# Optimization experiments

Hardware: AMD Instinct MI355X
Metric: run time of the kernel (lower is better)

Reference implementation:

```python
import jax, jax.numpy as jnp
import numpy as np
from jax import lax

B, T, V, H, L = 4096, 256, 256, 20, 15  # batch, seq_len, one_hot_size, hidden_dim, MAX_LABEL


def setup_inputs() -> dict:
    key = jax.random.key(0)
    k0, k1, k2, k3 = jax.random.split(key, 4)
    return {
        "x": jax.random.randint(k0, (B, T), 0, V, dtype=jnp.int32),
        "drop_rate": jnp.float32(0.0),
        "kernel": jax.random.normal(k1, (V, 3 * H), dtype=jnp.float32) * 0.05,
        "recurrent_kernel": jax.random.normal(k2, (H, 3 * H), dtype=jnp.float32) * 0.05,
        "bias": jnp.zeros((2, 3 * H), dtype=jnp.float32),  # [input_bias, recurrent_bias] (reset_after=True)
        "dense_w": jax.random.normal(k3, (H, L), dtype=jnp.float32) * 0.05,
        "dense_b": jnp.zeros((L,), dtype=jnp.float32),
    }


def reference(x, drop_rate, kernel, recurrent_kernel, bias, dense_w, dense_b):
    # one_hot(x, 256) @ kernel is exactly a row-gather of kernel: same math, no 1GB one-hot.
    bi, br = bias[0], bias[1]
    xW = kernel[x] + bi  # [B, T, 3H]

    def step(h, xw_t):
        # Keras GRUCell, reset_after=True, gate order (z, r, h)
        hU = h @ recurrent_kernel + br                      # [B, 3H]
        xz, xr, xh = jnp.split(xw_t, 3, axis=-1)
        hz, hr, hh = jnp.split(hU, 3, axis=-1)
        z = jax.nn.sigmoid(xz + hz)
        r = jax.nn.sigmoid(xr + hr)
        h_cand = jnp.tanh(xh + r * hh)
        h_new = z * h + (1.0 - z) * h_cand
        return h_new, None

    h0 = jnp.zeros((x.shape[0], recurrent_kernel.shape[0]), dtype=kernel.dtype)
    hT, _ = lax.scan(step, h0, jnp.swapaxes(xW, 0, 1))     # scan over time, final state [B, H]

    # tf.nn.dropout: keep with prob 1-rate, scale kept values by 1/(1-rate).
    keep = 1.0 - drop_rate
    mask = jax.random.uniform(jax.random.key(42), hT.shape) >= drop_rate
    h_drop = jnp.where(mask, hT / keep, 0.0)

    logits = h_drop @ dense_w + dense_b                     # [B, 15]
    return logits
```

## Files before the change

### kernel.cpp

```cpp
#include <hip/hip_runtime.h>


#define BB 4096
#define TT 256
#define VV 256
#define HH 20
#define G3 60
#define LL 15
#define L2E 1.44269504088896340736f

typedef int v4i __attribute__((ext_vector_type(4)));
typedef int v2i __attribute__((ext_vector_type(2)));

static __device__ __forceinline__ unsigned short f2bf(float f) {
    union { float f; unsigned int i; } c; c.f = f;
    unsigned int x = c.i;
    return (unsigned short)((x + 0x7FFFu + ((x >> 16) & 1u)) >> 16);
}
static __device__ __forceinline__ unsigned pack2bf(float a, float b) {
    return (unsigned)f2bf(a) | ((unsigned)f2bf(b) << 16);
}
static __device__ __forceinline__ float fast_rcp(float x) {
#if __has_builtin(__builtin_amdgcn_rcpf)
    return __builtin_amdgcn_rcpf(x);
#else
    return 1.0f / x;
#endif
}
static __device__ __forceinline__ float dot2bf(unsigned a, unsigned b, float c) {
    float d;
    asm("v_dot2_f32_bf16 %0, %1, %2, %3" : "=v"(d) : "v"(a), "v"(b), "v"(c));
    return d;
}
static __device__ __forceinline__ unsigned cvtpk(float a, float b) {
    unsigned r;
    asm("v_cvt_pk_bf16_f32 %0, %1, %2" : "=v"(r) : "v"(a), "v"(b));
    return r;
}
static __device__ __forceinline__ float exp2i(float x) {
    float r; asm("v_exp_f32 %0, %1" : "=v"(r) : "v"(x)); return r;
}
static __device__ __forceinline__ void h_exchange(unsigned waddr, unsigned hbf,
                                                  unsigned raddr,
                                                  v4i& p0, v4i& p1, v2i& p2) {
    asm volatile(
        "ds_write_b16 %3, %4\n\t"
        "ds_read_b128 %0, %5\n\t"
        "ds_read_b128 %1, %5 offset:16\n\t"
        "ds_read_b64 %2, %5 offset:32\n\t"
        "s_waitcnt lgkmcnt(0)"
        : "=&v"(p0), "=&v"(p1), "=&v"(p2)
        : "v"(waddr), "v"(hbf), "v"(raddr));
}

__global__ __launch_bounds__(64, 2) void gru_kernel(
    const int* __restrict__ x,
    const float* __restrict__ kernelW,
    const float* __restrict__ rkernel,
    const float* __restrict__ bias,
    const float* __restrict__ dense_w,
    const float* __restrict__ dense_b,
    float* __restrict__ out)
{
    __shared__ __align__(16) unsigned short hbuf[80];

    const int lane = threadIdx.x;
    const int g3a  = lane / 20;
    const int g3   = (lane < 60) ? g3a : 0;
    const int j    = lane - g3a * 20;
    const bool active = (lane < 60);
    const long b  = (long)blockIdx.x * 3 + g3;
    const long bc = (b < BB) ? b : (BB - 1);

    if (lane < 40) *(int*)&hbuf[lane * 2] = 0;

    const unsigned hbase = (unsigned)(size_t)&hbuf[0];
    const unsigned waddr = active ? (hbase + 48u * (unsigned)g3a + 2u * (unsigned)j)
                                  : (hbase + 144u + 2u * (unsigned)(lane - 60));
    const unsigned raddr = hbase + 48u * (unsigned)g3;

    unsigned Uz[10], Ur[10], Uh[10];
    #pragma unroll
    for (int q = 0; q < 10; ++q) {
        Uz[q] = pack2bf(rkernel[(2*q)*G3 + j]        * (-L2E),
                        rkernel[(2*q+1)*G3 + j]      * (-L2E));
        Ur[q] = pack2bf(rkernel[(2*q)*G3 + HH + j]   * (-L2E),
                        rkernel[(2*q+1)*G3 + HH + j] * (-L2E));
        Uh[q] = pack2bf(rkernel[(2*q)*G3 + 2*HH + j]   * (2.0f*L2E),
                        rkernel[(2*q+1)*G3 + 2*HH + j] * (2.0f*L2E));
    }
    const float bzc = (bias[j]        + bias[G3 + j])      * (-L2E);
    const float brc = (bias[HH + j]   + bias[G3 + HH + j]) * (-L2E);
    const float bhi =  bias[2*HH + j]                      * (2.0f*L2E);
    const float brh =  bias[G3 + 2*HH + j]                 * (2.0f*L2E);

    const int* xrow = x + bc * TT;

    const int xv0 = xrow[0];
    const float* kw0 = kernelW + xv0 * G3;
    float cz = fmaf(kw0[j],        -L2E,     bzc);
    float cr = fmaf(kw0[HH + j],   -L2E,     brc);
    float ch = fmaf(kw0[2*HH + j], 2.0f*L2E, bhi);
    int xvA = xrow[1];

    float hmine = 0.0f;
    unsigned hbf = 0;

    for (int t = 0; t < TT; ++t) {
        const float* kwn = kernelW + xvA * G3;
        const float lz = kwn[j];
        const float lr = kwn[HH + j];
        const float lh = kwn[2*HH + j];
        const int xvB = xrow[(t + 2 < TT) ? (t + 2) : (TT - 1)];

        v4i p0, p1; v2i p2;
        h_exchange(waddr, hbf, raddr, p0, p1, p2);
        const unsigned hp[10] = { (unsigned)p0.x, (unsigned)p0.y, (unsigned)p0.z,
                                  (unsigned)p0.w, (unsigned)p1.x, (unsigned)p1.y,
                                  (unsigned)p1.z, (unsigned)p1.w, (unsigned)p2.x,
                                  (unsigned)p2.y };

        float za = cz,  ra = cr,  ha = brh;
        float zb = 0.f, rb = 0.f, hb = 0.f;
        #pragma unroll
        for (int q = 0; q < 5; ++q) {
            za = dot2bf(hp[q], Uz[q], za);
            ra = dot2bf(hp[q], Ur[q], ra);
            ha = dot2bf(hp[q], Uh[q], ha);
        }
        #pragma unroll
        for (int q = 5; q < 10; ++q) {
            zb = dot2bf(hp[q], Uz[q], zb);
            rb = dot2bf(hp[q], Ur[q], rb);
            hb = dot2bf(hp[q], Uh[q], hb);
        }

        const float z  = fast_rcp(1.0f + exp2i(za + zb));
        const float r  = fast_rcp(1.0f + exp2i(ra + rb));
        const float yh = fmaf(r, ha + hb, ch);
        const float hc = fmaf(-2.0f, fast_rcp(1.0f + exp2i(yh)), 1.0f);
        hmine = hc + z * (hmine - hc);
        hbf = cvtpk(hmine, hmine);

        cz = fmaf(lz, -L2E,     bzc);
        cr = fmaf(lr, -L2E,     brc);
        ch = fmaf(lh, 2.0f*L2E, bhi);
        xvA = xvB;
    }

    v4i p0, p1; v2i p2;
    h_exchange(waddr, hbf, raddr, p0, p1, p2);
    const unsigned fp[10] = { (unsigned)p0.x, (unsigned)p0.y, (unsigned)p0.z,
                              (unsigned)p0.w, (unsigned)p1.x, (unsigned)p1.y,
                              (unsigned)p1.z, (unsigned)p1.w, (unsigned)p2.x,
                              (unsigned)p2.y };
    float hf[HH];
    #pragma unroll
    for (int q = 0; q < 10; ++q) {
        hf[2*q]   = __uint_as_float(fp[q] << 16);
        hf[2*q+1] = __uint_as_float(fp[q] & 0xffff0000u);
    }

    if (active && j < LL && b < BB) {
        float acc = dense_b[j];
        #pragma unroll
        for (int i = 0; i < HH; ++i)
            acc = fmaf(hf[i], dense_w[i * LL + j], acc);
        out[b * LL + j] = acc;
    }
}

extern "C" void kernel_launch(void* const* d_in, const int* in_sizes, int n_in,
                              void* d_out, int out_size, void* d_ws, size_t ws_size,
                              hipStream_t stream) {
    const int* x            = (const int*)d_in[0];
    const float* kernelW    = (const float*)d_in[2];
    const float* rkernel    = (const float*)d_in[3];
    const float* bias       = (const float*)d_in[4];
    const float* dense_w    = (const float*)d_in[5];
    const float* dense_b    = (const float*)d_in[6];
    float* out              = (float*)d_out;

    dim3 grid((BB + 2) / 3);
    dim3 block(64);
    gru_kernel<<<grid, block, 0, stream>>>(x, kernelW, rkernel, bias,
                                           dense_w, dense_b, out);
}
```

Measured before the change: 83.40 us.

## Map one sequence per wave and exchange hidden state via DPP/readlane

After: 147.4 us. 76.8% more time.

```diff
diff --git a/kernel.cpp b/kernel.cpp
--- a/kernel.cpp
+++ b/kernel.cpp
@@ -8,9 +8,6 @@
 #define G3 60
 #define LL 15
 #define L2E 1.44269504088896340736f
-
-typedef int v4i __attribute__((ext_vector_type(4)));
-typedef int v2i __attribute__((ext_vector_type(2)));
 
 static __device__ __forceinline__ unsigned short f2bf(float f) {
     union { float f; unsigned int i; } c; c.f = f;
@@ -27,33 +24,21 @@
     return 1.0f / x;
 #endif
 }
-static __device__ __forceinline__ float dot2bf(unsigned a, unsigned b, float c) {
+static __device__ __forceinline__ float dot2bf_s(unsigned a, unsigned b, float c) {
     float d;
-    asm("v_dot2_f32_bf16 %0, %1, %2, %3" : "=v"(d) : "v"(a), "v"(b), "v"(c));
+    asm("v_dot2_f32_bf16 %0, %1, %2, %3" : "=v"(d) : "s"(a), "v"(b), "v"(c));
     return d;
 }
-static __device__ __forceinline__ unsigned cvtpk(float a, float b) {
+static __device__ __forceinline__ unsigned cvtpk(float lo, float hi) {
     unsigned r;
-    asm("v_cvt_pk_bf16_f32 %0, %1, %2" : "=v"(r) : "v"(a), "v"(b));
+    asm("v_cvt_pk_bf16_f32 %0, %1, %2" : "=v"(r) : "v"(lo), "v"(hi));
     return r;
 }
 static __device__ __forceinline__ float exp2i(float x) {
     float r; asm("v_exp_f32 %0, %1" : "=v"(r) : "v"(x)); return r;
 }
-static __device__ __forceinline__ void h_exchange(unsigned waddr, unsigned hbf,
-                                                  unsigned raddr,
-                                                  v4i& p0, v4i& p1, v2i& p2) {
-    asm volatile(
-        "ds_write_b16 %3, %4\n\t"
-        "ds_read_b128 %0, %5\n\t"
-        "ds_read_b128 %1, %5 offset:16\n\t"
-        "ds_read_b64 %2, %5 offset:32\n\t"
-        "s_waitcnt lgkmcnt(0)"
-        : "=&v"(p0), "=&v"(p1), "=&v"(p2)
-        : "v"(waddr), "v"(hbf), "v"(raddr));
-}
 
-__global__ __launch_bounds__(64, 2) void gru_kernel(
+__global__ __launch_bounds__(64, 4) void gru_kernel(
     const int* __restrict__ x,
     const float* __restrict__ kernelW,
     const float* __restrict__ rkernel,
@@ -62,22 +47,9 @@
     const float* __restrict__ dense_b,
     float* __restrict__ out)
 {
-    __shared__ __align__(16) unsigned short hbuf[80];
-
     const int lane = threadIdx.x;
-    const int g3a  = lane / 20;
-    const int g3   = (lane < 60) ? g3a : 0;
-    const int j    = lane - g3a * 20;
-    const bool active = (lane < 60);
-    const long b  = (long)blockIdx.x * 3 + g3;
-    const long bc = (b < BB) ? b : (BB - 1);
-
-    if (lane < 40) *(int*)&hbuf[lane * 2] = 0;
-
-    const unsigned hbase = (unsigned)(size_t)&hbuf[0];
-    const unsigned waddr = active ? (hbase + 48u * (unsigned)g3a + 2u * (unsigned)j)
-                                  : (hbase + 144u + 2u * (unsigned)(lane - 60));
-    const unsigned raddr = hbase + 48u * (unsigned)g3;
+    const int j = (lane < HH) ? lane : 0;
+    const long b = blockIdx.x;
 
     unsigned Uz[10], Ur[10], Uh[10];
     #pragma unroll
@@ -94,7 +66,7 @@
     const float bhi =  bias[2*HH + j]                      * (2.0f*L2E);
     const float brh =  bias[G3 + 2*HH + j]                 * (2.0f*L2E);
 
-    const int* xrow = x + bc * TT;
+    const int* xrow = x + b * TT;
 
     const int xv0 = xrow[0];
     const float* kw0 = kernelW + xv0 * G3;
@@ -103,8 +75,7 @@
     float ch = fmaf(kw0[2*HH + j], 2.0f*L2E, bhi);
     int xvA = xrow[1];
 
-    float hmine = 0.0f;
-    unsigned hbf = 0;
+    float hm = 0.0f;
 
     for (int t = 0; t < TT; ++t) {
         const float* kwn = kernelW + xvA * G3;
@@ -113,34 +84,34 @@
         const float lh = kwn[2*HH + j];
         const int xvB = xrow[(t + 2 < TT) ? (t + 2) : (TT - 1)];
 
-        v4i p0, p1; v2i p2;
-        h_exchange(waddr, hbf, raddr, p0, p1, p2);
-        const unsigned hp[10] = { (unsigned)p0.x, (unsigned)p0.y, (unsigned)p0.z,
-                                  (unsigned)p0.w, (unsigned)p1.x, (unsigned)p1.y,
-                                  (unsigned)p1.z, (unsigned)p1.w, (unsigned)p2.x,
-                                  (unsigned)p2.y };
+        const int partner = __builtin_amdgcn_update_dpp(
+            0, __float_as_int(hm), 0xB1, 0xF, 0xF, true);
+        const unsigned pk = cvtpk(hm, __int_as_float(partner));
+        unsigned hp[10];
+        #pragma unroll
+        for (int q = 0; q < 10; ++q)
+            hp[q] = (unsigned)__builtin_amdgcn_readlane((int)pk, 2 * q);
 
         float za = cz,  ra = cr,  ha = brh;
         float zb = 0.f, rb = 0.f, hb = 0.f;
         #pragma unroll
         for (int q = 0; q < 5; ++q) {
-            za = dot2bf(hp[q], Uz[q], za);
-            ra = dot2bf(hp[q], Ur[q], ra);
-            ha = dot2bf(hp[q], Uh[q], ha);
+            za = dot2bf_s(hp[q], Uz[q], za);
+            ra = dot2bf_s(hp[q], Ur[q], ra);
+            ha = dot2bf_s(hp[q], Uh[q], ha);
         }
         #pragma unroll
         for (int q = 5; q < 10; ++q) {
-            zb = dot2bf(hp[q], Uz[q], zb);
-            rb = dot2bf(hp[q], Ur[q], rb);
-            hb = dot2bf(hp[q], Uh[q], hb);
+            zb = dot2bf_s(hp[q], Uz[q], zb);
+            rb = dot2bf_s(hp[q], Ur[q], rb);
+            hb = dot2bf_s(hp[q], Uh[q], hb);
         }
 
         const float z  = fast_rcp(1.0f + exp2i(za + zb));
         const float r  = fast_rcp(1.0f + exp2i(ra + rb));
         const float yh = fmaf(r, ha + hb, ch);
         const float hc = fmaf(-2.0f, fast_rcp(1.0f + exp2i(yh)), 1.0f);
-        hmine = hc + z * (hmine - hc);
-        hbf = cvtpk(hmine, hmine);
+        hm = hc + z * (hm - hc);
 
         cz = fmaf(lz, -L2E,     bzc);
         cr = fmaf(lr, -L2E,     brc);
@@ -148,25 +119,26 @@
         xvA = xvB;
     }
 
-    v4i p0, p1; v2i p2;
-    h_exchange(waddr, hbf, raddr, p0, p1, p2);
-    const unsigned fp[10] = { (unsigned)p0.x, (unsigned)p0.y, (unsigned)p0.z,
-                              (unsigned)p0.w, (unsigned)p1.x, (unsigned)p1.y,
-                              (unsigned)p1.z, (unsigned)p1.w, (unsigned)p2.x,
-                              (unsigned)p2.y };
-    float hf[HH];
+    const int partner = __builtin_amdgcn_update_dpp(
+        0, __float_as_int(hm), 0xB1, 0xF, 0xF, true);
+    const unsigned pk = cvtpk(hm, __int_as_float(partner));
+    unsigned hf[10];
     #pragma unroll
-    for (int q = 0; q < 10; ++q) {
-        hf[2*q]   = __uint_as_float(fp[q] << 16);
-        hf[2*q+1] = __uint_as_float(fp[q] & 0xffff0000u);
-    }
+    for (int q = 0; q < 10; ++q)
+        hf[q] = (unsigned)__builtin_amdgcn_readlane((int)pk, 2 * q);
 
-    if (active && j < LL && b < BB) {
-        float acc = dense_b[j];
+    if (lane < LL) {
+        float acc = dense_b[lane];
         #pragma unroll
-        for (int i = 0; i < HH; ++i)
-            acc = fmaf(hf[i], dense_w[i * LL + j], acc);
-        out[b * LL + j] = acc;
+        for (int q = 0; q < 10; ++q) {
+            const unsigned wp = pack2bf(dense_w[(2*q) * LL + lane],
+                                        dense_w[(2*q+1) * LL + lane]);
+            float d;
+            asm("v_dot2_f32_bf16 %0, %1, %2, %3"
+                : "=v"(d) : "s"(hf[q]), "v"(wp), "v"(acc));
+            acc = d;
+        }
+        out[b * LL + lane] = acc;
     }
 }
 
@@ -181,7 +153,7 @@
     const float* dense_b    = (const float*)d_in[6];
     float* out              = (float*)d_out;
 
-    dim3 grid((BB + 2) / 3);
+    dim3 grid(BB);
     dim3 block(64);
     gru_kernel<<<grid, block, 0, stream>>>(x, kernelW, rkernel, bias,
                                            dense_w, dense_b, out);
```

## Replace LDS hidden-state exchange with DPP pair packing and ds_bpermute

Applied to the files above, without the earlier changes.

Result: slower. 92.03 us (+10.3%).

```diff
diff --git a/kernel.cpp b/kernel.cpp
--- a/kernel.cpp
+++ b/kernel.cpp
@@ -8,9 +8,6 @@
 #define G3 60
 #define LL 15
 #define L2E 1.44269504088896340736f
-
-typedef int v4i __attribute__((ext_vector_type(4)));
-typedef int v2i __attribute__((ext_vector_type(2)));
 
 static __device__ __forceinline__ unsigned short f2bf(float f) {
     union { float f; unsigned int i; } c; c.f = f;
@@ -32,28 +29,37 @@
     asm("v_dot2_f32_bf16 %0, %1, %2, %3" : "=v"(d) : "v"(a), "v"(b), "v"(c));
     return d;
 }
-static __device__ __forceinline__ unsigned cvtpk(float a, float b) {
+static __device__ __forceinline__ unsigned cvtpk(float lo, float hi) {
     unsigned r;
-    asm("v_cvt_pk_bf16_f32 %0, %1, %2" : "=v"(r) : "v"(a), "v"(b));
+    asm("v_cvt_pk_bf16_f32 %0, %1, %2" : "=v"(r) : "v"(lo), "v"(hi));
     return r;
 }
 static __device__ __forceinline__ float exp2i(float x) {
     float r; asm("v_exp_f32 %0, %1" : "=v"(r) : "v"(x)); return r;
 }
-static __device__ __forceinline__ void h_exchange(unsigned waddr, unsigned hbf,
-                                                  unsigned raddr,
-                                                  v4i& p0, v4i& p1, v2i& p2) {
+
+static __device__ __forceinline__ void bperm_x10(
+    unsigned pk, const int* __restrict__ ba, unsigned* __restrict__ hp) {
     asm volatile(
-        "ds_write_b16 %3, %4\n\t"
-        "ds_read_b128 %0, %5\n\t"
-        "ds_read_b128 %1, %5 offset:16\n\t"
-        "ds_read_b64 %2, %5 offset:32\n\t"
+        "ds_bpermute_b32 %0, %10, %20\n\t"
+        "ds_bpermute_b32 %1, %11, %20\n\t"
+        "ds_bpermute_b32 %2, %12, %20\n\t"
+        "ds_bpermute_b32 %3, %13, %20\n\t"
+        "ds_bpermute_b32 %4, %14, %20\n\t"
+        "ds_bpermute_b32 %5, %15, %20\n\t"
+        "ds_bpermute_b32 %6, %16, %20\n\t"
+        "ds_bpermute_b32 %7, %17, %20\n\t"
+        "ds_bpermute_b32 %8, %18, %20\n\t"
+        "ds_bpermute_b32 %9, %19, %20\n\t"
         "s_waitcnt lgkmcnt(0)"
-        : "=&v"(p0), "=&v"(p1), "=&v"(p2)
-        : "v"(waddr), "v"(hbf), "v"(raddr));
+        : "=&v"(hp[0]), "=&v"(hp[1]), "=&v"(hp[2]), "=&v"(hp[3]), "=&v"(hp[4]),
+          "=&v"(hp[5]), "=&v"(hp[6]), "=&v"(hp[7]), "=&v"(hp[8]), "=&v"(hp[9])
+        : "v"(ba[0]), "v"(ba[1]), "v"(ba[2]), "v"(ba[3]), "v"(ba[4]),
+          "v"(ba[5]), "v"(ba[6]), "v"(ba[7]), "v"(ba[8]), "v"(ba[9]),
+          "v"(pk));
 }
 
-__global__ __launch_bounds__(64, 2) void gru_kernel(
+__global__ __launch_bounds__(64, 4) void gru_kernel(
     const int* __restrict__ x,
     const float* __restrict__ kernelW,
     const float* __restrict__ rkernel,
@@ -62,8 +68,6 @@
     const float* __restrict__ dense_b,
     float* __restrict__ out)
 {
-    __shared__ __align__(16) unsigned short hbuf[80];
-
     const int lane = threadIdx.x;
     const int g3a  = lane / 20;
     const int g3   = (lane < 60) ? g3a : 0;
@@ -72,12 +76,9 @@
     const long b  = (long)blockIdx.x * 3 + g3;
     const long bc = (b < BB) ? b : (BB - 1);
 
-    if (lane < 40) *(int*)&hbuf[lane * 2] = 0;
-
-    const unsigned hbase = (unsigned)(size_t)&hbuf[0];
-    const unsigned waddr = active ? (hbase + 48u * (unsigned)g3a + 2u * (unsigned)j)
-                                  : (hbase + 144u + 2u * (unsigned)(lane - 60));
-    const unsigned raddr = hbase + 48u * (unsigned)g3;
+    int ba[10];
+    #pragma unroll
+    for (int q = 0; q < 10; ++q) ba[q] = (g3 * 20 + 2 * q) * 4;
 
     unsigned Uz[10], Ur[10], Uh[10];
     #pragma unroll
@@ -103,8 +104,8 @@
     float ch = fmaf(kw0[2*HH + j], 2.0f*L2E, bhi);
     int xvA = xrow[1];
 
-    float hmine = 0.0f;
-    unsigned hbf = 0;
+    float hm = 0.0f;
+    unsigned pk = 0;
 
     for (int t = 0; t < TT; ++t) {
         const float* kwn = kernelW + xvA * G3;
@@ -113,12 +114,8 @@
         const float lh = kwn[2*HH + j];
         const int xvB = xrow[(t + 2 < TT) ? (t + 2) : (TT - 1)];
 
-        v4i p0, p1; v2i p2;
-        h_exchange(waddr, hbf, raddr, p0, p1, p2);
-        const unsigned hp[10] = { (unsigned)p0.x, (unsigned)p0.y, (unsigned)p0.z,
-                                  (unsigned)p0.w, (unsigned)p1.x, (unsigned)p1.y,
-                                  (unsigned)p1.z, (unsigned)p1.w, (unsigned)p2.x,
-                                  (unsigned)p2.y };
+        unsigned hp[10];
+        bperm_x10(pk, ba, hp);
 
         float za = cz,  ra = cr,  ha = brh;
         float zb = 0.f, rb = 0.f, hb = 0.f;
@@ -139,8 +136,11 @@
         const float r  = fast_rcp(1.0f + exp2i(ra + rb));
         const float yh = fmaf(r, ha + hb, ch);
         const float hc = fmaf(-2.0f, fast_rcp(1.0f + exp2i(yh)), 1.0f);
-        hmine = hc + z * (hmine - hc);
-        hbf = cvtpk(hmine, hmine);
+        hm = hc + z * (hm - hc);
+
+        const int partner = __builtin_amdgcn_update_dpp(
+            0, __float_as_int(hm), 0xB1, 0xF, 0xF, true);
+        pk = cvtpk(hm, __int_as_float(partner));
 
         cz = fmaf(lz, -L2E,     bzc);
         cr = fmaf(lr, -L2E,     brc);
@@ -148,12 +148,8 @@
         xvA = xvB;
     }
 
-    v4i p0, p1; v2i p2;
-    h_exchange(waddr, hbf, raddr, p0, p1, p2);
-    const unsigned fp[10] = { (unsigned)p0.x, (unsigned)p0.y, (unsigned)p0.z,
-                              (unsigned)p0.w, (unsigned)p1.x, (unsigned)p1.y,
-                              (unsigned)p1.z, (unsigned)p1.w, (unsigned)p2.x,
-                              (unsigned)p2.y };
+    unsigned fp[10];
+    bperm_x10(pk, ba, fp);
     float hf[HH];
     #pragma unroll
     for (int q = 0; q < 10; ++q) {
```
